# Kernel tuning notes

Hardware: AMD Instinct MI355X
Metric: run time of the kernel (lower is better)

Reference implementation:

```python
import jax, jax.numpy as jnp
import numpy as np

# Episode constants (match init_kwargs / input shapes)
B, WAY, SHOT, K = 2, 5, 5, 5
Q_NUM, DIM, HW = 30, 64, 441
BN_EPS = 1e-5


def _episode(q, s, gamma, beta, w3):
    """q: [Q, D, HW] query features; s: [WAY*SHOT, D, HW] support features."""
    # --- cosine logits between mean-pooled query and class prototypes ---
    q_pool = q.mean(axis=2)                                        # [Q, D]
    proto = s.mean(axis=2).reshape(WAY, SHOT, DIM).mean(axis=1)    # [WAY, D]
    qF = q_pool / jnp.linalg.norm(q_pool, axis=-1, keepdims=True)
    pF = proto / jnp.linalg.norm(proto, axis=-1, keepdims=True)
    logits_cos = qF @ pF.T                                         # [Q, WAY]

    # --- spatially L2-normalized descriptors (norm over HW axis, as in torch) ---
    q_norm = q / jnp.linalg.norm(q, axis=2, keepdims=True)         # [Q, D, HW]
    s_norm = s / jnp.linalg.norm(s, axis=2, keepdims=True)         # [WAY*SHOT, D, HW]
    s_l = s_norm.reshape(WAY, SHOT * DIM, HW)                      # [WAY, S*D, HW]
    s_p = jnp.transpose(s_norm, (0, 2, 1)).reshape(WAY, SHOT * HW, DIM)  # [WAY, S*HW, D]

    # channel-level similarity: [Q, WAY, D, SHOT*D], top-k over last axis
    ip_l = jnp.einsum('qdh,wkh->qwdk', q_norm, s_l)
    top_l, _ = jax.lax.top_k(ip_l, K)
    sim_l = top_l.sum(axis=(2, 3))                                 # [Q, WAY]

    # pixel-level similarity: [Q, WAY, HW, SHOT*HW], top-k over last axis
    ip_p = jnp.einsum('qhd,wkd->qwhk', jnp.transpose(q_norm, (0, 2, 1)), s_p)
    top_p, _ = jax.lax.top_k(ip_p, K)
    sim_p = top_p.sum(axis=(2, 3))                                 # [Q, WAY]

    # --- BatchNorm1d(3*WAY), training mode (per-episode batch stats) ---
    feats = jnp.concatenate([logits_cos, sim_l, sim_p], axis=1)    # [Q, 3*WAY]
    mu = feats.mean(axis=0)
    var = feats.var(axis=0)  # biased, as torch BN uses for normalization
    feats_bn = (feats - mu) / jnp.sqrt(var + BN_EPS) * gamma + beta

    # --- Conv1d(1,1,kernel=3,dilation=5,no bias): out length 3*WAY-10 ---
    L = 3 * WAY
    out = w3[0] * feats_bn[:, :L - 10] + w3[1] * feats_bn[:, 5:L - 5] + w3[2] * feats_bn[:, 10:]
    return out                                                      # [Q, WAY]


def setup_inputs() -> dict:
    key = jax.random.key(0)
    k1, k2, k3 = jax.random.split(key, 3)
    return {
        'input1_batch': jax.random.normal(k1, (B * Q_NUM, DIM, HW), dtype=jnp.float32),
        'input2_batch': jax.random.normal(k2, (B * WAY * SHOT, DIM, HW), dtype=jnp.float32),
        'gamma': jnp.ones((3 * WAY,), dtype=jnp.float32),
        'beta': jnp.zeros((3 * WAY,), dtype=jnp.float32),
        'conv_w': jax.random.normal(k3, (1, 1, 3), dtype=jnp.float32),
    }


def reference(input1_batch, input2_batch, gamma, beta, conv_w):
    q = input1_batch.reshape(B, Q_NUM, DIM, HW)
    s = input2_batch.reshape(B, WAY * SHOT, DIM, HW)
    w3 = conv_w.reshape(3)
    sim = jax.vmap(lambda qi, si: _episode(qi, si, gamma, beta, w3))(q, s)
    return sim  # [B, Q_NUM, WAY]
```

## Files before the change

### kernel.cpp

```cpp
#include <hip/hip_runtime.h>
#include <math.h>


typedef __attribute__((ext_vector_type(8))) short bf16x8;
typedef __attribute__((ext_vector_type(4))) float f32x4;

#define MFMA16(a, b, c) __builtin_amdgcn_mfma_f32_16x16x32_bf16((a), (b), (c), 0, 0, 0)

__device__ __forceinline__ unsigned short to_bf16(float v) {
    unsigned int u = __float_as_uint(v);
    unsigned int r = u + 0x7FFFu + ((u >> 16) & 1u);
    return (unsigned short)(r >> 16);
}

__device__ __forceinline__ void ins5(float m[5], float v) {
    m[4] = __builtin_amdgcn_fmed3f(v, m[4], m[3]);
    m[3] = __builtin_amdgcn_fmed3f(v, m[3], m[2]);
    m[2] = __builtin_amdgcn_fmed3f(v, m[2], m[1]);
    m[1] = __builtin_amdgcn_fmed3f(v, m[1], m[0]);
    m[0] = fmaxf(m[0], v);
}

__global__ __launch_bounds__(256) void k1_rownorm(const float* __restrict__ in1,
                                                  const float* __restrict__ in2,
                                                  float* __restrict__ inv_norm,
                                                  float* __restrict__ pool) {
    int wv = threadIdx.x >> 6;
    int lane = threadIdx.x & 63;
    int rid = blockIdx.x * 4 + wv;
    const float* src = (rid < 3840) ? (in1 + (size_t)rid * 441)
                                    : (in2 + (size_t)(rid - 3840) * 441);
    float s = 0.f, ss = 0.f;
#pragma unroll
    for (int i = 0; i < 7; ++i) {
        int h = lane + i * 64;
        if (h < 441) { float v = src[h]; s += v; ss = fmaf(v, v, ss); }
    }
#pragma unroll
    for (int off = 32; off > 0; off >>= 1) {
        s += __shfl_xor(s, off, 64);
        ss += __shfl_xor(ss, off, 64);
    }
    if (lane == 0) {
        inv_norm[rid] = 1.0f / sqrtf(ss);
        pool[rid] = s * (1.0f / 441.0f);
    }
}

__global__ __launch_bounds__(256, 4) void pack_all(const float* __restrict__ in1,
                                                   const float* __restrict__ in2,
                                                   const float* __restrict__ inv_norm,
                                                   const float* __restrict__ pool,
                                                   uint4* __restrict__ Pq,
                                                   uint4* __restrict__ Ps,
                                                   uint4* __restrict__ Al,
                                                   uint4* __restrict__ Bl,
                                                   float* __restrict__ feats) {
    int bid = blockIdx.x;
    int tid = threadIdx.x;
    unsigned short hs[8];
    if (bid < 840) {
        int idx = bid * 256 + tid;
        int lane = idx & 63;
        int ks = (idx >> 6) & 1;
        int rest = idx >> 7;
        int gcs = rest % 840, e = rest / 840;
        int q = gcs / 28, cs = gcs % 28;
        int h = cs * 16 + (lane & 15);
        int d0 = ks * 32 + ((lane >> 4) << 3);
        int rowq = (e * 30 + q) * 64;
#pragma unroll
        for (int j = 0; j < 8; ++j) {
            int d = d0 + j;
            float v = (h < 441) ? in1[(size_t)(rowq + d) * 441 + h] * inv_norm[rowq + d] : 0.f;
            hs[j] = to_bf16(v);
        }
        uint4 H;
        H.x = hs[0] | (hs[1] << 16); H.y = hs[2] | (hs[3] << 16);
        H.z = hs[4] | (hs[5] << 16); H.w = hs[6] | (hs[7] << 16);
        Pq[idx] = H;
    } else if (bid < 1530) {
        int idx = (bid - 840) * 256 + tid;
        int lane = idx & 63;
        int ks = (idx >> 6) & 1;
        int rest = idx >> 7;
        int kt = rest % 138, ew = rest / 138;
        int kidx = kt * 16 + (lane & 15);
        bool valid = kidx < 2205;
        int kc = valid ? kidx : 0;
        int sh = kc / 441;
        int h = kc - sh * 441;
        int e = ew / 5, w = ew % 5;
        int srow = ((e * 25 + w * 5 + sh) * 64);
        int d0 = ks * 32 + ((lane >> 4) << 3);
#pragma unroll
        for (int j = 0; j < 8; ++j) {
            int d = d0 + j;
            float v = valid ? in2[(size_t)(srow + d) * 441 + h] * inv_norm[3840 + srow + d] : 0.f;
            hs[j] = to_bf16(v);
        }
        uint4 H;
        H.x = hs[0] | (hs[1] << 16); H.y = hs[2] | (hs[3] << 16);
        H.z = hs[4] | (hs[5] << 16); H.w = hs[6] | (hs[7] << 16);
        Ps[idx] = H;
    } else if (bid < 2230) {
        int idx = (bid - 1530) * 256 + tid;
        int lane = idx & 63;
        int t2 = idx >> 6;
        int ks = t2 % 14;
        int t3 = t2 / 14;
        int rt = t3 % 20, ew = t3 / 20;
        int e = ew / 5, w = ew % 5;
        int row = rt * 16 + (lane & 15);
        int sh = row >> 6, dp = row & 63;
        int srow = (e * 25 + w * 5 + sh) * 64 + dp;
        int h0 = ks * 32 + ((lane >> 4) << 3);
        const float* src = in2 + (size_t)srow * 441;
        float inv = inv_norm[3840 + srow];
#pragma unroll
        for (int j = 0; j < 8; ++j) {
            int h = h0 + j;
            float v = (h < 441) ? src[h] * inv : 0.f;
            hs[j] = to_bf16(v);
        }
        uint4 H;
        H.x = hs[0] | (hs[1] << 16); H.y = hs[2] | (hs[3] << 16);
        H.z = hs[4] | (hs[5] << 16); H.w = hs[6] | (hs[7] << 16);
        Al[idx] = H;
    } else if (bid < 3070) {
        int idx = (bid - 2230) * 256 + tid;
        int lane = idx & 63;
        int t2 = idx >> 6;
        int ks = t2 % 14;
        int t3 = t2 / 14;
        int gct = t3 % 120, e = t3 / 120;
        int col = gct * 16 + (lane & 15);
        int q = col >> 6, d = col & 63;
        int qrow = (e * 30 + q) * 64 + d;
        int h0 = ks * 32 + ((lane >> 4) << 3);
        const float* src = in1 + (size_t)qrow * 441;
        float inv = inv_norm[qrow];
#pragma unroll
        for (int j = 0; j < 8; ++j) {
            int h = h0 + j;
            float v = (h < 441) ? src[h] * inv : 0.f;
            hs[j] = to_bf16(v);
        }
        uint4 H;
        H.x = hs[0] | (hs[1] << 16); H.y = hs[2] | (hs[3] << 16);
        H.z = hs[4] | (hs[5] << 16); H.w = hs[6] | (hs[7] << 16);
        Bl[idx] = H;
    } else {
        int e = bid - 3070;
        __shared__ float qp[30 * 64], pr[5 * 64], qn[30], pn[5];
        int t = tid;
        for (int li = t; li < 1920; li += 256) qp[li] = pool[e * 30 * 64 + li];
        for (int li = t; li < 320; li += 256) {
            int w = li >> 6, d = li & 63;
            float sm = 0.f;
            for (int sh = 0; sh < 5; ++sh) sm += pool[(60 + e * 25 + w * 5 + sh) * 64 + d];
            pr[li] = sm * 0.2f;
        }
        __syncthreads();
        if (t < 30) {
            float ss = 0.f;
            for (int d = 0; d < 64; ++d) { float v = qp[t * 64 + d]; ss = fmaf(v, v, ss); }
            qn[t] = 1.0f / sqrtf(ss);
        }
        if (t >= 32 && t < 37) {
            int w = t - 32; float ss = 0.f;
            for (int d = 0; d < 64; ++d) { float v = pr[w * 64 + d]; ss = fmaf(v, v, ss); }
            pn[w] = 1.0f / sqrtf(ss);
        }
        __syncthreads();
        if (t < 150) {
            int q = t / 5, w = t % 5;
            float dp = 0.f;
            for (int d = 0; d < 64; ++d) dp = fmaf(qp[q * 64 + d], pr[w * 64 + d], dp);
            feats[(e * 30 + q) * 15 + w] = dp * qn[q] * pn[w];
        }
    }
}

template <int NRR>
__device__ __forceinline__ void chan_pass(int rr0, int ew, int e, int q, int wv, int lane,
                                          const bf16x8* __restrict__ Bl,
                                          const bf16x8* __restrict__ Al,
                                          float m[4][5]) {
    f32x4 cc[NRR][4];
#pragma unroll
    for (int r = 0; r < NRR; ++r)
#pragma unroll
        for (int s = 0; s < 4; ++s) cc[r][s] = (f32x4){0.f, 0.f, 0.f, 0.f};
    for (int ks = 0; ks < 14; ++ks) {
        bf16x8 bh[4];
#pragma unroll
        for (int s = 0; s < 4; ++s)
            bh[s] = Bl[((e * 120 + q * 4 + s) * 14 + ks) * 64 + lane];
#pragma unroll
        for (int r = 0; r < NRR; ++r) {
            bf16x8 ah = Al[((ew * 20 + wv * 5 + rr0 + r) * 14 + ks) * 64 + lane];
#pragma unroll
            for (int s = 0; s < 4; ++s) cc[r][s] = MFMA16(ah, bh[s], cc[r][s]);
        }
    }
#pragma unroll
    for (int r = 0; r < NRR; ++r)
#pragma unroll
        for (int s = 0; s < 4; ++s)
#pragma unroll
            for (int g = 0; g < 4; ++g) ins5(m[s], cc[r][s][g]);
}

__global__ __launch_bounds__(256, 2) void k56(const bf16x8* __restrict__ Pq,
                                              const uint4* __restrict__ PsU4,
                                              const bf16x8* __restrict__ Bl,
                                              const bf16x8* __restrict__ Al,
                                              float* __restrict__ part_p,
                                              float* __restrict__ siml) {
    __shared__ uint4 SB[1024];
    int bid = blockIdx.x;
    int tid = threadIdx.x;
    int xcd = bid & 7;
    int slot = bid >> 3;
    int wv = tid >> 6, lane = tid & 63;
    const f32x4 ZV = {0.f, 0.f, 0.f, 0.f};

    if (slot < 67) {
        int p = xcd * 67 + slot;
        if (p >= 530) return;
        int ew = p / 53;
        int blk = p - ew * 53;
        int e = ew / 5, w = ew - (ew / 5) * 5;
        int gwave = blk * 4 + wv;
        bool act = gwave < 210;
        int gv = act ? gwave : 209;
        int q = gv / 7;
        int ct0 = gv * 4;

        bf16x8 Bh[4][2];
#pragma unroll
        for (int s = 0; s < 4; ++s)
#pragma unroll
            for (int ks = 0; ks < 2; ++ks)
                Bh[s][ks] = ((const bf16x8*)Pq)[((e * 840 + ct0 + s) * 2 + ks) * 64 + lane];

        float m[4][5];
#pragma unroll
        for (int s = 0; s < 4; ++s)
#pragma unroll
            for (int i = 0; i < 5; ++i) m[s][i] = -1e30f;

        int rowbase = (lane >> 4) * 4;
        const uint4* g = PsU4 + (size_t)ew * 138 * 128;
        const bf16x8* SBf = (const bf16x8*)SB;

        {
            uint4 r0 = g[tid], r1 = g[tid + 256];
            SB[tid] = r0; SB[tid + 256] = r1;
        }
        __syncthreads();

        for (int c = 0; c < 34; ++c) {
            uint4 r0 = g[(size_t)(c + 1) * 512 + tid];
            uint4 r1 = g[(size_t)(c + 1) * 512 + 256 + tid];
            int rb = (c & 1) * 512;
            if (act) {
#pragma unroll
                for (int j = 0; j < 4; ++j) {
                    bf16x8 a0 = SBf[rb + j * 128 + lane];
                    bf16x8 a1 = SBf[rb + j * 128 + 64 + lane];
#pragma unroll
                    for (int s = 0; s < 4; ++s) {
                        f32x4 cv = MFMA16(a0, Bh[s][0], ZV);
                        cv = MFMA16(a1, Bh[s][1], cv);
#pragma unroll
                        for (int gg = 0; gg < 4; ++gg) ins5(m[s], cv[gg]);
                    }
                }
            }
            int wb = ((c + 1) & 1) * 512;
            SB[wb + tid] = r0; SB[wb + 256 + tid] = r1;
            __syncthreads();
        }
        if (act) {
            {
                bf16x8 a0 = SBf[0 * 128 + lane];
                bf16x8 a1 = SBf[0 * 128 + 64 + lane];
#pragma unroll
                for (int s = 0; s < 4; ++s) {
                    f32x4 cv = MFMA16(a0, Bh[s][0], ZV);
                    cv = MFMA16(a1, Bh[s][1], cv);
#pragma unroll
                    for (int gg = 0; gg < 4; ++gg) ins5(m[s], cv[gg]);
                }
            }
            {
                bf16x8 a0 = SBf[1 * 128 + lane];
                bf16x8 a1 = SBf[1 * 128 + 64 + lane];
#pragma unroll
                for (int s = 0; s < 4; ++s) {
                    f32x4 cv = MFMA16(a0, Bh[s][0], ZV);
                    cv = MFMA16(a1, Bh[s][1], cv);
#pragma unroll
                    for (int gg = 0; gg < 4; ++gg) {
                        float v = (rowbase + gg < 13) ? cv[gg] : -1e30f;
                        ins5(m[s], v);
                    }
                }
            }

#pragma unroll
            for (int mask = 16; mask <= 32; mask <<= 1) {
                float ov[4][5];
#pragma unroll
                for (int s = 0; s < 4; ++s)
#pragma unroll
                    for (int i = 0; i < 5; ++i) ov[s][i] = __shfl_xor(m[s][i], mask, 64);
#pragma unroll
                for (int s = 0; s < 4; ++s)
#pragma unroll
                    for (int i = 0; i < 5; ++i) ins5(m[s], ov[s][i]);
            }

            float tot = 0.f;
#pragma unroll
            for (int s = 0; s < 4; ++s) {
                float s5 = m[s][0] + m[s][1] + m[s][2] + m[s][3] + m[s][4];
                int h = ((ct0 + s) % 28) * 16 + (lane & 15);
                s5 = (h < 441) ? s5 : 0.f;
#pragma unroll
                for (int mask = 1; mask <= 8; mask <<= 1) s5 += __shfl_xor(s5, mask, 64);
                tot += s5;
            }
            if (lane == 0) {
                int sl = gv - q * 7;
                part_p[((e * 30 + q) * 5 + w) * 7 + sl] = tot;
            }
        }
    } else {
        float (*Mred)[64][5] = (float (*)[64][5])SB;
        int c = xcd * 38 + (slot - 67);
        if (c >= 300) return;
        int ew = c / 30, q = c - ew * 30;
        int e = ew / 5, w = ew - (ew / 5) * 5;

        float m[4][5];
#pragma unroll
        for (int s = 0; s < 4; ++s)
#pragma unroll
            for (int i = 0; i < 5; ++i) m[s][i] = -1e30f;

        chan_pass<3>(0, ew, e, q, wv, lane, Bl, Al, m);
        chan_pass<2>(3, ew, e, q, wv, lane, Bl, Al, m);

#pragma unroll
        for (int mask = 16; mask <= 32; mask <<= 1) {
            float ov[4][5];
#pragma unroll
            for (int s = 0; s < 4; ++s)
#pragma unroll
                for (int i = 0; i < 5; ++i) ov[s][i] = __shfl_xor(m[s][i], mask, 64);
#pragma unroll
            for (int s = 0; s < 4; ++s)
#pragma unroll
                for (int i = 0; i < 5; ++i) ins5(m[s], ov[s][i]);
        }

        if (lane < 16) {
#pragma unroll
            for (int s = 0; s < 4; ++s)
#pragma unroll
                for (int i = 0; i < 5; ++i) Mred[wv][s * 16 + lane][i] = m[s][i];
        }
        __syncthreads();

        if (tid < 64) {
            float lst[5];
#pragma unroll
            for (int i = 0; i < 5; ++i) lst[i] = Mred[0][tid][i];
#pragma unroll
            for (int v2 = 1; v2 < 4; ++v2)
#pragma unroll
                for (int i = 0; i < 5; ++i) ins5(lst, Mred[v2][tid][i]);
            float s5 = lst[0] + lst[1] + lst[2] + lst[3] + lst[4];
#pragma unroll
            for (int mask = 1; mask <= 32; mask <<= 1) s5 += __shfl_xor(s5, mask, 64);
            if (tid == 0) siml[(e * 30 + q) * 5 + w] = s5;
        }
    }
}

__global__ __launch_bounds__(256) void k7_final(const float* __restrict__ feats,
                                                const float* __restrict__ siml,
                                                const float* __restrict__ part_p,
                                                const float* __restrict__ gamma,
                                                const float* __restrict__ beta,
                                                const float* __restrict__ convw,
                                                float* __restrict__ out) {
    int e = blockIdx.x;
    __shared__ float f[30 * 15], mu[15], inv[15];
    int t = threadIdx.x;
    if (t < 150) {
        int q = t / 5, w = t % 5;
        int pb = ((e * 30 + q) * 5 + w) * 7;
        float sp = 0.f;
#pragma unroll
        for (int s = 0; s < 7; ++s) sp += part_p[pb + s];
        f[q * 15 + w] = feats[(e * 30 + q) * 15 + w];
        f[q * 15 + 5 + w] = siml[(e * 30 + q) * 5 + w];
        f[q * 15 + 10 + w] = sp;
    }
    __syncthreads();
    if (t < 15) {
        float s1 = 0.f;
        for (int q = 0; q < 30; ++q) s1 += f[q * 15 + t];
        float mn = s1 * (1.0f / 30.0f);
        float s2 = 0.f;
        for (int q = 0; q < 30; ++q) { float d = f[q * 15 + t] - mn; s2 = fmaf(d, d, s2); }
        mu[t] = mn;
        inv[t] = 1.0f / sqrtf(s2 * (1.0f / 30.0f) + 1e-5f);
    }
    __syncthreads();
    if (t < 150) {
        int q = t / 5, j = t % 5;
        float w0 = convw[0], w1 = convw[1], w2 = convw[2];
        float b0 = (f[q * 15 + j]      - mu[j])      * inv[j]      * gamma[j]      + beta[j];
        float b1 = (f[q * 15 + 5 + j]  - mu[5 + j])  * inv[5 + j]  * gamma[5 + j]  + beta[5 + j];
        float b2 = (f[q * 15 + 10 + j] - mu[10 + j]) * inv[10 + j] * gamma[10 + j] + beta[10 + j];
        out[e * 150 + q * 5 + j] = w0 * b0 + w1 * b1 + w2 * b2;
    }
}

extern "C" void kernel_launch(void* const* d_in, const int* in_sizes, int n_in,
                              void* d_out, int out_size, void* d_ws, size_t ws_size,
                              hipStream_t stream) {
    const float* in1 = (const float*)d_in[0];
    const float* in2 = (const float*)d_in[1];
    const float* gamma = (const float*)d_in[2];
    const float* beta = (const float*)d_in[3];
    const float* convw = (const float*)d_in[4];
    float* out = (float*)d_out;

    char* ws = (char*)d_ws;
    float* inv_norm = (float*)(ws + 0);
    float* pool     = (float*)(ws + 28160);
    float* feats    = (float*)(ws + 56320);
    float* siml     = (float*)(ws + 59920);
    float* part_p   = (float*)(ws + 61120);
    size_t o = 69520;
    uint4* Pq = (uint4*)(ws + o); o += 3440640;
    uint4* Ps = (uint4*)(ws + o); o += 2826240;
    uint4* Al = (uint4*)(ws + o); o += 2867200;
    uint4* Bl = (uint4*)(ws + o); o += 3440640;

    k1_rownorm<<<dim3(1760), dim3(256), 0, stream>>>(in1, in2, inv_norm, pool);
    pack_all<<<dim3(3072), dim3(256), 0, stream>>>(in1, in2, inv_norm, pool,
                                                   Pq, Ps, Al, Bl, feats);
    k56<<<dim3(840), dim3(256), 0, stream>>>((const bf16x8*)Pq, Ps,
                                             (const bf16x8*)Bl, (const bf16x8*)Al,
                                             part_p, siml);
    k7_final<<<dim3(2), dim3(256), 0, stream>>>(feats, siml, part_p, gamma, beta, convw, out);
}
```

Before: 127.1 us.

## Split fused pixel/channel kernel into two kernels with one column tile per wave

The combined k56 kernel is split into a pixel-level kernel (k6_pix) and a channel-level kernel (k5_chan). In k6_pix each wave now handles a single 16-column query tile instead of four, so the grid grows to 2100 blocks with launch bounds of 6 blocks per CU for higher occupancy. Partial results widen to 28 slots per (e,q,w), and the final kernel and workspace offsets change to match. The cost is that each support chunk is streamed into LDS by four times as many blocks, plus an extra kernel launch that serialises the channel work after the pixel work.

```diff
diff --git a/kernel.cpp b/kernel.cpp
--- a/kernel.cpp
+++ b/kernel.cpp
@@ -182,42 +182,9 @@
     }
 }
 
-template <int NRR>
-__device__ __forceinline__ void chan_pass(int rr0, int ew, int e, int q, int wv, int lane,
-                                          const bf16x8* __restrict__ Bl,
-                                          const bf16x8* __restrict__ Al,
-                                          float m[4][5]) {
-    f32x4 cc[NRR][4];
-#pragma unroll
-    for (int r = 0; r < NRR; ++r)
-#pragma unroll
-        for (int s = 0; s < 4; ++s) cc[r][s] = (f32x4){0.f, 0.f, 0.f, 0.f};
-    for (int ks = 0; ks < 14; ++ks) {
-        bf16x8 bh[4];
-#pragma unroll
-        for (int s = 0; s < 4; ++s)
-            bh[s] = Bl[((e * 120 + q * 4 + s) * 14 + ks) * 64 + lane];
-#pragma unroll
-        for (int r = 0; r < NRR; ++r) {
-            bf16x8 ah = Al[((ew * 20 + wv * 5 + rr0 + r) * 14 + ks) * 64 + lane];
-#pragma unroll
-            for (int s = 0; s < 4; ++s) cc[r][s] = MFMA16(ah, bh[s], cc[r][s]);
-        }
-    }
-#pragma unroll
-    for (int r = 0; r < NRR; ++r)
-#pragma unroll
-        for (int s = 0; s < 4; ++s)
-#pragma unroll
-            for (int g = 0; g < 4; ++g) ins5(m[s], cc[r][s][g]);
-}
-
-__global__ __launch_bounds__(256, 2) void k56(const bf16x8* __restrict__ Pq,
-                                              const uint4* __restrict__ PsU4,
-                                              const bf16x8* __restrict__ Bl,
-                                              const bf16x8* __restrict__ Al,
-                                              float* __restrict__ part_p,
-                                              float* __restrict__ siml) {
+__global__ __launch_bounds__(256, 6) void k6_pix(const bf16x8* __restrict__ Pq,
+                                                 const uint4* __restrict__ PsU4,
+                                                 float* __restrict__ part_p) {
     __shared__ uint4 SB[1024];
     int bid = blockIdx.x;
     int tid = threadIdx.x;
@@ -226,168 +193,172 @@
     int wv = tid >> 6, lane = tid & 63;
     const f32x4 ZV = {0.f, 0.f, 0.f, 0.f};
 
-    if (slot < 67) {
-        int p = xcd * 67 + slot;
-        if (p >= 530) return;
-        int ew = p / 53;
-        int blk = p - ew * 53;
-        int e = ew / 5, w = ew - (ew / 5) * 5;
-        int gwave = blk * 4 + wv;
-        bool act = gwave < 210;
-        int gv = act ? gwave : 209;
-        int q = gv / 7;
-        int ct0 = gv * 4;
-
-        bf16x8 Bh[4][2];
+    int p = xcd * 263 + slot;
+    if (p >= 2100) return;
+    int ew = p / 210;
+    int gwave = p - ew * 210;
+    int e = ew / 5, w = ew - (ew / 5) * 5;
+    int q = gwave / 7;
+    int cs = gwave * 4 + wv;
+
+    bf16x8 Bh0 = Pq[((e * 840 + cs) * 2 + 0) * 64 + lane];
+    bf16x8 Bh1 = Pq[((e * 840 + cs) * 2 + 1) * 64 + lane];
+
+    float m[5];
+#pragma unroll
+    for (int i = 0; i < 5; ++i) m[i] = -1e30f;
+
+    int rowbase = (lane >> 4) * 4;
+    const uint4* g = PsU4 + (size_t)ew * 138 * 128;
+    const bf16x8* SBf = (const bf16x8*)SB;
+
+    {
+        uint4 r0 = g[tid], r1 = g[tid + 256];
+        SB[tid] = r0; SB[tid + 256] = r1;
+    }
+    __syncthreads();
+
+    for (int c = 0; c < 34; ++c) {
+        uint4 r0 = g[(size_t)(c + 1) * 512 + tid];
+        uint4 r1 = g[(size_t)(c + 1) * 512 + 256 + tid];
+        int rb = (c & 1) * 512;
+#pragma unroll
+        for (int j = 0; j < 4; ++j) {
+            bf16x8 a0 = SBf[rb + j * 128 + lane];
+            bf16x8 a1 = SBf[rb + j * 128 + 64 + lane];
+            f32x4 cv = MFMA16(a0, Bh0, ZV);
+            cv = MFMA16(a1, Bh1, cv);
+            ins5(m, cv[0]); ins5(m, cv[1]); ins5(m, cv[2]); ins5(m, cv[3]);
+        }
+        int wb = ((c + 1) & 1) * 512;
+        SB[wb + tid] = r0; SB[wb + 256 + tid] = r1;
+        __syncthreads();
+    }
+    {
+        bf16x8 a0 = SBf[0 * 128 + lane];
+        bf16x8 a1 = SBf[0 * 128 + 64 + lane];
+        f32x4 cv = MFMA16(a0, Bh0, ZV);
+        cv = MFMA16(a1, Bh1, cv);
+        ins5(m, cv[0]); ins5(m, cv[1]); ins5(m, cv[2]); ins5(m, cv[3]);
+
+        a0 = SBf[1 * 128 + lane];
+        a1 = SBf[1 * 128 + 64 + lane];
+        cv = MFMA16(a0, Bh0, ZV);
+        cv = MFMA16(a1, Bh1, cv);
+#pragma unroll
+        for (int gg = 0; gg < 4; ++gg) {
+            float v = (rowbase + gg < 13) ? cv[gg] : -1e30f;
+            ins5(m, v);
+        }
+    }
+
+#pragma unroll
+    for (int mask = 16; mask <= 32; mask <<= 1) {
+        float ov[5];
+#pragma unroll
+        for (int i = 0; i < 5; ++i) ov[i] = __shfl_xor(m[i], mask, 64);
+#pragma unroll
+        for (int i = 0; i < 5; ++i) ins5(m, ov[i]);
+    }
+
+    float s5 = m[0] + m[1] + m[2] + m[3] + m[4];
+    int h = (cs % 28) * 16 + (lane & 15);
+    s5 = (h < 441) ? s5 : 0.f;
+#pragma unroll
+    for (int mask = 1; mask <= 8; mask <<= 1) s5 += __shfl_xor(s5, mask, 64);
+    if (lane == 0) {
+        int sl = gwave - q * 7;
+        part_p[((e * 30 + q) * 5 + w) * 28 + sl * 4 + wv] = s5;
+    }
+}
+
+template <int NRR>
+__device__ __forceinline__ void chan_pass(int rr0, int ew, int e, int q, int wv, int lane,
+                                          const bf16x8* __restrict__ Bl,
+                                          const bf16x8* __restrict__ Al,
+                                          float m[4][5]) {
+    f32x4 cc[NRR][4];
+#pragma unroll
+    for (int r = 0; r < NRR; ++r)
+#pragma unroll
+        for (int s = 0; s < 4; ++s) cc[r][s] = (f32x4){0.f, 0.f, 0.f, 0.f};
+    for (int ks = 0; ks < 14; ++ks) {
+        bf16x8 bh[4];
 #pragma unroll
         for (int s = 0; s < 4; ++s)
-#pragma unroll
-            for (int ks = 0; ks < 2; ++ks)
-                Bh[s][ks] = ((const bf16x8*)Pq)[((e * 840 + ct0 + s) * 2 + ks) * 64 + lane];
-
-        float m[4][5];
+            bh[s] = Bl[((e * 120 + q * 4 + s) * 14 + ks) * 64 + lane];
+#pragma unroll
+        for (int r = 0; r < NRR; ++r) {
+            bf16x8 ah = Al[((ew * 20 + wv * 5 + rr0 + r) * 14 + ks) * 64 + lane];
+#pragma unroll
+            for (int s = 0; s < 4; ++s) cc[r][s] = MFMA16(ah, bh[s], cc[r][s]);
+        }
+    }
+#pragma unroll
+    for (int r = 0; r < NRR; ++r)
 #pragma unroll
         for (int s = 0; s < 4; ++s)
 #pragma unroll
-            for (int i = 0; i < 5; ++i) m[s][i] = -1e30f;
-
-        int rowbase = (lane >> 4) * 4;
-        const uint4* g = PsU4 + (size_t)ew * 138 * 128;
-        const bf16x8* SBf = (const bf16x8*)SB;
-
-        {
-            uint4 r0 = g[tid], r1 = g[tid + 256];
-            SB[tid] = r0; SB[tid + 256] = r1;
-        }
-        __syncthreads();
-
-        for (int c = 0; c < 34; ++c) {
-            uint4 r0 = g[(size_t)(c + 1) * 512 + tid];
-            uint4 r1 = g[(size_t)(c + 1) * 512 + 256 + tid];
-            int rb = (c & 1) * 512;
-            if (act) {
-#pragma unroll
-                for (int j = 0; j < 4; ++j) {
-                    bf16x8 a0 = SBf[rb + j * 128 + lane];
-                    bf16x8 a1 = SBf[rb + j * 128 + 64 + lane];
-#pragma unroll
-                    for (int s = 0; s < 4; ++s) {
-                        f32x4 cv = MFMA16(a0, Bh[s][0], ZV);
-                        cv = MFMA16(a1, Bh[s][1], cv);
-#pragma unroll
-                        for (int gg = 0; gg < 4; ++gg) ins5(m[s], cv[gg]);
-                    }
-                }
-            }
-            int wb = ((c + 1) & 1) * 512;
-            SB[wb + tid] = r0; SB[wb + 256 + tid] = r1;
-            __syncthreads();
-        }
-        if (act) {
-            {
-                bf16x8 a0 = SBf[0 * 128 + lane];
-                bf16x8 a1 = SBf[0 * 128 + 64 + lane];
-#pragma unroll
-                for (int s = 0; s < 4; ++s) {
-                    f32x4 cv = MFMA16(a0, Bh[s][0], ZV);
-                    cv = MFMA16(a1, Bh[s][1], cv);
-#pragma unroll
-                    for (int gg = 0; gg < 4; ++gg) ins5(m[s], cv[gg]);
-                }
-            }
-            {
-                bf16x8 a0 = SBf[1 * 128 + lane];
-                bf16x8 a1 = SBf[1 * 128 + 64 + lane];
-#pragma unroll
-                for (int s = 0; s < 4; ++s) {
-                    f32x4 cv = MFMA16(a0, Bh[s][0], ZV);
-                    cv = MFMA16(a1, Bh[s][1], cv);
-#pragma unroll
-                    for (int gg = 0; gg < 4; ++gg) {
-                        float v = (rowbase + gg < 13) ? cv[gg] : -1e30f;
-                        ins5(m[s], v);
-                    }
-                }
-            }
-
-#pragma unroll
-            for (int mask = 16; mask <= 32; mask <<= 1) {
-                float ov[4][5];
-#pragma unroll
-                for (int s = 0; s < 4; ++s)
-#pragma unroll
-                    for (int i = 0; i < 5; ++i) ov[s][i] = __shfl_xor(m[s][i], mask, 64);
-#pragma unroll
-                for (int s = 0; s < 4; ++s)
-#pragma unroll
-                    for (int i = 0; i < 5; ++i) ins5(m[s], ov[s][i]);
-            }
-
-            float tot = 0.f;
-#pragma unroll
-            for (int s = 0; s < 4; ++s) {
-                float s5 = m[s][0] + m[s][1] + m[s][2] + m[s][3] + m[s][4];
-                int h = ((ct0 + s) % 28) * 16 + (lane & 15);
-                s5 = (h < 441) ? s5 : 0.f;
-#pragma unroll
-                for (int mask = 1; mask <= 8; mask <<= 1) s5 += __shfl_xor(s5, mask, 64);
-                tot += s5;
-            }
-            if (lane == 0) {
-                int sl = gv - q * 7;
-                part_p[((e * 30 + q) * 5 + w) * 7 + sl] = tot;
-            }
-        }
-    } else {
-        float (*Mred)[64][5] = (float (*)[64][5])SB;
-        int c = xcd * 38 + (slot - 67);
-        if (c >= 300) return;
-        int ew = c / 30, q = c - ew * 30;
-        int e = ew / 5, w = ew - (ew / 5) * 5;
-
-        float m[4][5];
+            for (int g = 0; g < 4; ++g) ins5(m[s], cc[r][s][g]);
+}
+
+__global__ __launch_bounds__(256, 2) void k5_chan(const bf16x8* __restrict__ Bl,
+                                                  const bf16x8* __restrict__ Al,
+                                                  float* __restrict__ siml) {
+    __shared__ float Mred[4][64][5];
+    int bid = blockIdx.x;
+    int tid = threadIdx.x;
+    int xcd = bid & 7;
+    int slot = bid >> 3;
+    int wv = tid >> 6, lane = tid & 63;
+
+    int c = xcd * 38 + slot;
+    if (c >= 300) return;
+    int ew = c / 30, q = c - ew * 30;
+    int e = ew / 5, w = ew - (ew / 5) * 5;
+
+    float m[4][5];
+#pragma unroll
+    for (int s = 0; s < 4; ++s)
+#pragma unroll
+        for (int i = 0; i < 5; ++i) m[s][i] = -1e30f;
+
+    chan_pass<3>(0, ew, e, q, wv, lane, Bl, Al, m);
+    chan_pass<2>(3, ew, e, q, wv, lane, Bl, Al, m);
+
+#pragma unroll
+    for (int mask = 16; mask <= 32; mask <<= 1) {
+        float ov[4][5];
 #pragma unroll
         for (int s = 0; s < 4; ++s)
 #pragma unroll
-            for (int i = 0; i < 5; ++i) m[s][i] = -1e30f;
-
-        chan_pass<3>(0, ew, e, q, wv, lane, Bl, Al, m);
-        chan_pass<2>(3, ew, e, q, wv, lane, Bl, Al, m);
-
-#pragma unroll
-        for (int mask = 16; mask <= 32; mask <<= 1) {
-            float ov[4][5];
-#pragma unroll
-            for (int s = 0; s < 4; ++s)
-#pragma unroll
-                for (int i = 0; i < 5; ++i) ov[s][i] = __shfl_xor(m[s][i], mask, 64);
-#pragma unroll
-            for (int s = 0; s < 4; ++s)
-#pragma unroll
-                for (int i = 0; i < 5; ++i) ins5(m[s], ov[s][i]);
-        }
-
-        if (lane < 16) {
-#pragma unroll
-            for (int s = 0; s < 4; ++s)
-#pragma unroll
-                for (int i = 0; i < 5; ++i) Mred[wv][s * 16 + lane][i] = m[s][i];
-        }
-        __syncthreads();
-
-        if (tid < 64) {
-            float lst[5];
-#pragma unroll
-            for (int i = 0; i < 5; ++i) lst[i] = Mred[0][tid][i];
-#pragma unroll
-            for (int v2 = 1; v2 < 4; ++v2)
-#pragma unroll
-                for (int i = 0; i < 5; ++i) ins5(lst, Mred[v2][tid][i]);
-            float s5 = lst[0] + lst[1] + lst[2] + lst[3] + lst[4];
-#pragma unroll
-            for (int mask = 1; mask <= 32; mask <<= 1) s5 += __shfl_xor(s5, mask, 64);
-            if (tid == 0) siml[(e * 30 + q) * 5 + w] = s5;
-        }
+            for (int i = 0; i < 5; ++i) ov[s][i] = __shfl_xor(m[s][i], mask, 64);
+#pragma unroll
+        for (int s = 0; s < 4; ++s)
+#pragma unroll
+            for (int i = 0; i < 5; ++i) ins5(m[s], ov[s][i]);
+    }
+
+    if (lane < 16) {
+#pragma unroll
+        for (int s = 0; s < 4; ++s)
+#pragma unroll
+            for (int i = 0; i < 5; ++i) Mred[wv][s * 16 + lane][i] = m[s][i];
+    }
+    __syncthreads();
+
+    if (tid < 64) {
+        float lst[5];
+#pragma unroll
+        for (int i = 0; i < 5; ++i) lst[i] = Mred[0][tid][i];
+#pragma unroll
+        for (int v2 = 1; v2 < 4; ++v2)
+#pragma unroll
+            for (int i = 0; i < 5; ++i) ins5(lst, Mred[v2][tid][i]);
+        float s5 = lst[0] + lst[1] + lst[2] + lst[3] + lst[4];
+#pragma unroll
+        for (int mask = 1; mask <= 32; mask <<= 1) s5 += __shfl_xor(s5, mask, 64);
+        if (tid == 0) siml[(e * 30 + q) * 5 + w] = s5;
     }
 }
 
@@ -403,10 +374,10 @@
     int t = threadIdx.x;
     if (t < 150) {
         int q = t / 5, w = t % 5;
-        int pb = ((e * 30 + q) * 5 + w) * 7;
+        int pb = ((e * 30 + q) * 5 + w) * 28;
         float sp = 0.f;
 #pragma unroll
-        for (int s = 0; s < 7; ++s) sp += part_p[pb + s];
+        for (int s = 0; s < 28; ++s) sp += part_p[pb + s];
         f[q * 15 + w] = feats[(e * 30 + q) * 15 + w];
         f[q * 15 + 5 + w] = siml[(e * 30 + q) * 5 + w];
         f[q * 15 + 10 + w] = sp;
@@ -448,7 +419,7 @@
     float* feats    = (float*)(ws + 56320);
     float* siml     = (float*)(ws + 59920);
     float* part_p   = (float*)(ws + 61120);
-    size_t o = 69520;
+    size_t o = 128320;
     uint4* Pq = (uint4*)(ws + o); o += 3440640;
     uint4* Ps = (uint4*)(ws + o); o += 2826240;
     uint4* Al = (uint4*)(ws + o); o += 2867200;
@@ -457,8 +428,8 @@
     k1_rownorm<<<dim3(1760), dim3(256), 0, stream>>>(in1, in2, inv_norm, pool);
     pack_all<<<dim3(3072), dim3(256), 0, stream>>>(in1, in2, inv_norm, pool,
                                                    Pq, Ps, Al, Bl, feats);
-    k56<<<dim3(840), dim3(256), 0, stream>>>((const bf16x8*)Pq, Ps,
-                                             (const bf16x8*)Bl, (const bf16x8*)Al,
-                                             part_p, siml);
+    k6_pix<<<dim3(2104), dim3(256), 0, stream>>>((const bf16x8*)Pq, Ps, part_p);
+    k5_chan<<<dim3(304), dim3(256), 0, stream>>>((const bf16x8*)Bl, (const bf16x8*)Al,
+                                                 siml);
     k7_final<<<dim3(2), dim3(256), 0, stream>>>(feats, siml, part_p, gamma, beta, convw, out);
 }
```

New measurement: 132.5 us. 1.04x slower.
